# Kernel tuning notes

Hardware: AMD Instinct MI355X
Metric: run time of the kernel (lower is better)

Reference implementation:

```python
import jax, jax.numpy as jnp
import numpy as np

TAU = 1.5      # lif_tau
V_TH = 1.0     # spikingjelly default v_threshold
EPS = 1e-5     # BatchNorm eps
ALPHA = 4.0    # spikingjelly default sigmoid surrogate alpha

@jax.custom_vjp
def spike_fn(x):
    return (x >= 0.0).astype(x.dtype)

def _spike_fwd(x):
    return spike_fn(x), x

def _spike_bwd(x, g):
    s = jax.nn.sigmoid(ALPHA * x)
    return (g * ALPHA * s * (1.0 - s),)

spike_fn.defvjp(_spike_fwd, _spike_bwd)

def lif(x):
    # x: [T, B, C, N]; hard reset to 0, decay_input=True, detach_reset=True
    def step(v, xt):
        v = v + (xt - v) / TAU
        s = spike_fn(v - V_TH)
        sd = jax.lax.stop_gradient(s)
        v = (1.0 - sd) * v
        return v, s
    _, spikes = jax.lax.scan(step, jnp.zeros_like(x[0]), x)
    return spikes

def bn(x, gamma, beta, mean, var):
    # eval-mode BatchNorm1d over channel dim of [B, C, L]
    inv = gamma * jax.lax.rsqrt(var + EPS)
    return x * inv[None, :, None] + (beta - mean * inv)[None, :, None]

def setup_inputs() -> dict:
    key = jax.random.key(0)
    ks = jax.random.split(key, 13)
    B, C, T, N, H = 8, 256, 4, 4096, 1024
    return {
        "x": jax.random.normal(ks[0], (B, C, T, N), jnp.float32),
        "fc1_w": jax.random.normal(ks[1], (H, C), jnp.float32) * 0.05,
        "fc1_b": jax.random.normal(ks[2], (H,), jnp.float32) * 0.05,
        "fc2_w": jax.random.normal(ks[3], (C, H), jnp.float32) * 0.05,
        "fc2_b": jax.random.normal(ks[4], (C,), jnp.float32) * 0.05,
        "bn1_gamma": jax.random.uniform(ks[5], (H,), jnp.float32, 0.5, 1.5),
        "bn1_beta": jax.random.normal(ks[6], (H,), jnp.float32) * 0.1,
        "bn1_mean": jax.random.normal(ks[7], (H,), jnp.float32) * 0.1,
        "bn1_var": jax.random.uniform(ks[8], (H,), jnp.float32, 0.5, 1.5),
        "bn2_gamma": jax.random.uniform(ks[9], (C,), jnp.float32, 0.5, 1.5),
        "bn2_beta": jax.random.normal(ks[10], (C,), jnp.float32) * 0.1,
        "bn2_mean": jax.random.normal(ks[11], (C,), jnp.float32) * 0.1,
        "bn2_var": jax.random.uniform(ks[12], (C,), jnp.float32, 0.5, 1.5),
    }

def reference(x, fc1_w, fc1_b, fc2_w, fc2_b,
              bn1_gamma, bn1_beta, bn1_mean, bn1_var,
              bn2_gamma, bn2_beta, bn2_mean, bn2_var):
    B, C, T, N = x.shape
    H = fc1_w.shape[0]
    # fc2_bn on raw input, then LIF over T
    h = bn(x.reshape(B, C, T * N), bn2_gamma, bn2_beta, bn2_mean, bn2_var)
    h = h.reshape(B, C, T, N).transpose(2, 0, 1, 3)          # [T,B,C,N]
    h = lif(h).transpose(1, 2, 0, 3).reshape(B, C, T * N)    # [B,C,TN]
    # fc1: 1x1 conv == GEMM over channels
    h = jnp.einsum('hc,bcl->bhl', fc1_w, h) + fc1_b[None, :, None]
    h = bn(h, bn1_gamma, bn1_beta, bn1_mean, bn1_var)
    h = h.reshape(B, H, T, N).transpose(2, 0, 1, 3)          # [T,B,H,N]
    h = lif(h).transpose(1, 2, 0, 3).reshape(B, H, T * N)    # [B,H,TN]
    # fc2
    h = jnp.einsum('ch,bhl->bcl', fc2_w, h) + fc2_b[None, :, None]
    return h.reshape(B, C, T, N)
```

## Files before the change

kernel.cpp:

```cpp
#include <hip/hip_runtime.h>

#define BB 8
#define CC 256
#define TT 4
#define NNv 4096
#define HH 1024
#define LLv (TT*NNv)

typedef int int4v __attribute__((ext_vector_type(4)));

static __device__ __forceinline__ void barrier_keep_vmem() {
    asm volatile("s_waitcnt lgkmcnt(0)" ::: "memory");
    __builtin_amdgcn_s_barrier();
    __builtin_amdgcn_sched_barrier(0);
}

__global__ __launch_bounds__(256) void k_prep1(const float* __restrict__ w,
                                               unsigned char* __restrict__ wd)
{
    int i = blockIdx.x * 256 + threadIdx.x;
    int h = i >> 8, c = i & 255;
    int w24 = __float2int_rn(w[i] * 16777216.0f);
    int d2 = ((w24 + 128) & 255) - 128;  w24 = (w24 - d2) >> 8;
    int d1 = ((w24 + 128) & 255) - 128;  w24 = (w24 - d1) >> 8;
    int d0 = w24;
    size_t off = ((((size_t)(h >> 6) * 4 + (c >> 6)) * 4 + ((h >> 4) & 3)) << 10)
               + ((c >> 4) & 3) * 256 + (h & 15) * 16 + (c & 15);
    wd[off] = (unsigned char)d0;
    wd[262144 + off] = (unsigned char)d1;
    wd[2 * 262144 + off] = (unsigned char)d2;
}

__global__ __launch_bounds__(256) void k_prep2(const float* __restrict__ w,
                                               unsigned char* __restrict__ wd)
{
    int i = blockIdx.x * 256 + threadIdx.x;
    int c = i >> 10, h = i & 1023;
    int w16 = __float2int_rn(w[i] * 65536.0f);
    int d1 = ((w16 + 128) & 255) - 128;  w16 = (w16 - d1) >> 8;
    int d0 = w16;
    size_t off = ((((((size_t)(c >> 6) * 8 + (h >> 7)) * 2 + ((h >> 6) & 1)) * 4
                    + ((c >> 4) & 3)) << 10)
                 + ((h >> 4) & 3) * 256 + (c & 15) * 16 + (h & 15));
    wd[off] = (unsigned char)d0;
    wd[262144 + off] = (unsigned char)d1;
}

__global__ __launch_bounds__(256) void k_bn2_lif_t(
    const float* __restrict__ x,
    const float* __restrict__ g, const float* __restrict__ be,
    const float* __restrict__ mu, const float* __restrict__ va,
    unsigned char* __restrict__ s1T, int b0)
{
    __shared__ unsigned char ts[TT][64][80];
    int tx = threadIdx.x;
    int n0 = blockIdx.x * 64;
    int c0 = blockIdx.y * 64;
    int bl = blockIdx.z;
    int b  = b0 + bl;
    int cl = tx >> 2, np = tx & 3;
    int c = c0 + cl;
    float rsq = __fdiv_rn(1.0f, __fsqrt_rn(__fadd_rn(va[c], 1e-5f)));
    float inv = __fmul_rn(g[c], rsq);
    float add = __fsub_rn(be[c], __fmul_rn(mu[c], inv));
    size_t xb = ((size_t)(b * CC + c) * TT) * NNv + n0 + np * 16;
    float v[16];
    #pragma unroll
    for (int i = 0; i < 16; i++) v[i] = 0.0f;
    #pragma unroll
    for (int t = 0; t < TT; t++) {
        float4 p[4];
        #pragma unroll
        for (int k = 0; k < 4; k++) p[k] = *(const float4*)(x + xb + (size_t)t * NNv + 4 * k);
        const float* xp = (const float*)p;
        unsigned int ob[4] = {0, 0, 0, 0};
        #pragma unroll
        for (int i = 0; i < 16; i++) {
            float y = __fadd_rn(__fmul_rn(xp[i], inv), add);
            float vv = __fadd_rn(v[i], __fdiv_rn(__fsub_rn(y, v[i]), 1.5f));
            bool sp = vv >= 1.0f;
            v[i] = sp ? 0.0f : vv;
            if (sp) ob[i >> 2] |= 1u << (8 * (i & 3));
        }
        uint4 pk; pk.x = ob[0]; pk.y = ob[1]; pk.z = ob[2]; pk.w = ob[3];
        *(uint4*)&ts[t][cl][np * 16] = pk;
    }
    __syncthreads();
    int nl = tx >> 2, cp = tx & 3;
    #pragma unroll
    for (int t = 0; t < TT; t++) {
        unsigned int u[4];
        #pragma unroll
        for (int kk = 0; kk < 4; kk++) {
            u[kk] = (unsigned int)ts[t][cp * 16 + kk * 4 + 0][nl]
                  | ((unsigned int)ts[t][cp * 16 + kk * 4 + 1][nl] << 8)
                  | ((unsigned int)ts[t][cp * 16 + kk * 4 + 2][nl] << 16)
                  | ((unsigned int)ts[t][cp * 16 + kk * 4 + 3][nl] << 24);
        }
        uint4 pk; pk.x = u[0]; pk.y = u[1]; pk.z = u[2]; pk.w = u[3];
        *(uint4*)(s1T + ((size_t)(bl * TT + t) * NNv + n0 + nl) * CC + c0 + cp * 16) = pk;
    }
}

__global__ __launch_bounds__(256, 3) void k_gemm1_lif(
    const unsigned char* __restrict__ w1d,
    const float* __restrict__ b1,
    const float* __restrict__ g1, const float* __restrict__ be1,
    const float* __restrict__ mu1, const float* __restrict__ va1,
    const unsigned char* __restrict__ s1T, unsigned char* __restrict__ s2T)
{
    __shared__ unsigned char Lsraw[TT * 32 * 80];
    const int tx = threadIdx.x;
    const int n0 = blockIdx.x * 32;
    const int ht = blockIdx.y;
    const int bl = blockIdx.z;
    const int lane = tx & 63, w = tx >> 6;
    const int q = lane >> 4, ln = lane & 15;
    const int mh = (w & 1) * 32, wn = (w >> 1) * 16;
    const int h0 = ht * 64;

    int4v a0[TT][2], a1[TT][2], a2[TT][2];
    #pragma unroll
    for (int t = 0; t < TT; t++)
    #pragma unroll
    for (int mi = 0; mi < 2; mi++) {
        a0[t][mi] = (int4v){0, 0, 0, 0};
        a1[t][mi] = (int4v){0, 0, 0, 0};
        a2[t][mi] = (int4v){0, 0, 0, 0};
    }

    unsigned long long d[2][4];
    #pragma unroll
    for (int i = 0; i < 4; i++) {
        int task = i * 256 + tx;
        int cb = task & 7, nr = (task >> 3) & 31, t = task >> 8;
        d[0][i] = *(const unsigned long long*)(
            s1T + ((size_t)(bl * TT + t) * NNv + n0 + nr) * CC + 0 * 64 + cb * 8);
    }

    #pragma unroll
    for (int ko = 0; ko < 4; ko++) {
        const int cur = ko & 1;
        if (ko > 0) barrier_keep_vmem();
        #pragma unroll
        for (int i = 0; i < 4; i++) {
            int task = i * 256 + tx;
            int cb = task & 7, nr = (task >> 3) & 31, t = task >> 8;
            *(unsigned long long*)(Lsraw + (t * 32 + nr) * 80 + cb * 8) = d[cur][i];
        }
        if (ko < 3) {
            #pragma unroll
            for (int i = 0; i < 4; i++) {
                int task = i * 256 + tx;
                int cb = task & 7, nr = (task >> 3) & 31, t = task >> 8;
                d[cur ^ 1][i] = *(const unsigned long long*)(
                    s1T + ((size_t)(bl * TT + t) * NNv + n0 + nr) * CC + (ko + 1) * 64 + cb * 8);
            }
        }
        int4v w0[2], w1[2], w2[2];
        #pragma unroll
        for (int mi = 0; mi < 2; mi++) {
            size_t fb = ((((size_t)ht * 4 + ko) * 4 + (mh >> 4) + mi) << 10) + lane * 16;
            w0[mi] = *(const int4v*)(w1d + fb);
            w1[mi] = *(const int4v*)(w1d + 262144 + fb);
            w2[mi] = *(const int4v*)(w1d + 2 * 262144 + fb);
        }
        barrier_keep_vmem();

        int4v sf[TT];
        #pragma unroll
        for (int t = 0; t < TT; t++)
            sf[t] = *(const int4v*)(Lsraw + (t * 32 + wn + ln) * 80 + q * 16);
        #pragma unroll
        for (int t = 0; t < TT; t++)
        #pragma unroll
        for (int mi = 0; mi < 2; mi++) {
            a0[t][mi] = __builtin_amdgcn_mfma_i32_16x16x64_i8(w0[mi], sf[t], a0[t][mi], 0, 0, 0);
            a1[t][mi] = __builtin_amdgcn_mfma_i32_16x16x64_i8(w1[mi], sf[t], a1[t][mi], 0, 0, 0);
            a2[t][mi] = __builtin_amdgcn_mfma_i32_16x16x64_i8(w2[mi], sf[t], a2[t][mi], 0, 0, 0);
        }
    }

    barrier_keep_vmem();

    const int l_loc = wn + ln;
    #pragma unroll
    for (int mi = 0; mi < 2; mi++) {
        float invr[4], addr_[4], biasr[4];
        #pragma unroll
        for (int r = 0; r < 4; r++) {
            int h = h0 + mh + mi * 16 + q * 4 + r;
            float rsq = __fdiv_rn(1.0f, __fsqrt_rn(__fadd_rn(va1[h], 1e-5f)));
            invr[r] = __fmul_rn(g1[h], rsq);
            addr_[r] = __fsub_rn(be1[h], __fmul_rn(mu1[h], invr[r]));
            biasr[r] = b1[h];
        }
        float v4[4] = {0.f, 0.f, 0.f, 0.f};
        #pragma unroll
        for (int t = 0; t < TT; t++) {
            int4v ci = (((a0[t][mi] << 8) + a1[t][mi]) << 8) + a2[t][mi];
            unsigned int pk = 0;
            #pragma unroll
            for (int r = 0; r < 4; r++) {
                float h1 = __fadd_rn(__fmul_rn((float)ci[r], 5.9604644775390625e-08f),
                                     biasr[r]);
                float y  = __fadd_rn(__fmul_rn(h1, invr[r]), addr_[r]);
                float vv = __fadd_rn(v4[r], __fdiv_rn(__fsub_rn(y, v4[r]), 1.5f));
                bool sp = vv >= 1.0f;
                v4[r] = sp ? 0.0f : vv;
                if (sp) pk |= (1u << (8 * r));
            }
            *(unsigned int*)(Lsraw + (t * 32 + l_loc) * 80
                             + ((mh >> 2) + mi * 4 + q) * 4) = pk;
        }
    }
    __syncthreads();

    #pragma unroll
    for (int p = 0; p < 2; p++) {
        int task = p * 256 + tx;
        int t = task >> 7, l = (task >> 2) & 31, ch = task & 3;
        uint4 vv = *(const uint4*)(Lsraw + (t * 32 + l) * 80 + ch * 16);
        *(uint4*)(s2T + ((size_t)bl * LLv + t * NNv + n0 + l) * HH + h0 + ch * 16) = vv;
    }
}

__global__ __launch_bounds__(256, 3) void k_gemm2(
    const unsigned char* __restrict__ w2d,
    const float* __restrict__ b2c,
    const unsigned char* __restrict__ s2T, float* __restrict__ outp, int b0)
{
    __shared__ unsigned char Ls[64][144];
    const int tx = threadIdx.x;
    const int l0 = blockIdx.x * 64;
    const int ct = blockIdx.y;
    const int bl = blockIdx.z;
    const int b  = b0 + bl;
    const int lane = tx & 63, w = tx >> 6;
    const int q = lane >> 4, ln = lane & 15;
    const int mc = w * 32;

    int4v a0[2][4], a1[2][4];
    #pragma unroll
    for (int mi = 0; mi < 2; mi++)
    #pragma unroll
    for (int ni = 0; ni < 4; ni++) {
        a0[mi][ni] = (int4v){0, 0, 0, 0};
        a1[mi][ni] = (int4v){0, 0, 0, 0};
    }

    unsigned long long d[2][4];
    #pragma unroll
    for (int i = 0; i < 4; i++) {
        int task = i * 256 + tx;
        int hb = task & 15, lr = task >> 4;
        d[0][i] = *(const unsigned long long*)(
            s2T + ((size_t)bl * LLv + l0 + lr) * HH + 0 * 128 + hb * 8);
    }

    #pragma unroll
    for (int ko = 0; ko < 8; ko++) {
        const int cur = ko & 1;
        if (ko > 0) barrier_keep_vmem();
        #pragma unroll
        for (int i = 0; i < 4; i++) {
            int task = i * 256 + tx;
            int hb = task & 15, lr = task >> 4;
            *(unsigned long long*)&Ls[lr][hb * 8] = d[cur][i];
        }
        if (ko < 7) {
            #pragma unroll
            for (int i = 0; i < 4; i++) {
                int task = i * 256 + tx;
                int hb = task & 15, lr = task >> 4;
                d[cur ^ 1][i] = *(const unsigned long long*)(
                    s2T + ((size_t)bl * LLv + l0 + lr) * HH + (ko + 1) * 128 + hb * 8);
            }
        }
        int4v w0[2][2], w1[2][2];
        #pragma unroll
        for (int kb = 0; kb < 2; kb++)
        #pragma unroll
        for (int mi = 0; mi < 2; mi++) {
            size_t fb = (((((size_t)(ct * 2 + (w >> 1)) * 8 + ko) * 2 + kb) * 4
                          + (w & 1) * 2 + mi) << 10) + lane * 16;
            w0[kb][mi] = *(const int4v*)(w2d + fb);
            w1[kb][mi] = *(const int4v*)(w2d + 262144 + fb);
        }
        barrier_keep_vmem();

        #pragma unroll
        for (int kb = 0; kb < 2; kb++) {
            int4v sf[4];
            #pragma unroll
            for (int ni = 0; ni < 4; ni++)
                sf[ni] = *(const int4v*)&Ls[ni * 16 + ln][kb * 64 + q * 16];
            #pragma unroll
            for (int mi = 0; mi < 2; mi++)
            #pragma unroll
            for (int ni = 0; ni < 4; ni++) {
                a0[mi][ni] = __builtin_amdgcn_mfma_i32_16x16x64_i8(w0[kb][mi], sf[ni], a0[mi][ni], 0, 0, 0);
                a1[mi][ni] = __builtin_amdgcn_mfma_i32_16x16x64_i8(w1[kb][mi], sf[ni], a1[mi][ni], 0, 0, 0);
            }
        }
    }
    #pragma unroll
    for (int mi = 0; mi < 2; mi++)
    #pragma unroll
    for (int ni = 0; ni < 4; ni++) {
        int4v tv = (a0[mi][ni] << 8) + a1[mi][ni];
        #pragma unroll
        for (int r = 0; r < 4; r++) {
            int c = ct * 128 + mc + mi * 16 + q * 4 + r;
            int l = l0 + ni * 16 + ln;
            outp[((size_t)b * CC + c) * LLv + l] =
                __fadd_rn(__fmul_rn((float)tv[r], 1.52587890625e-05f), b2c[c]);
        }
    }
}

extern "C" void kernel_launch(void* const* d_in, const int* in_sizes, int n_in,
                              void* d_out, int out_size, void* d_ws, size_t ws_size,
                              hipStream_t stream) {
    const float* x    = (const float*)d_in[0];
    const float* fc1w = (const float*)d_in[1];
    const float* fc1b = (const float*)d_in[2];
    const float* fc2w = (const float*)d_in[3];
    const float* fc2b = (const float*)d_in[4];
    const float* g1   = (const float*)d_in[5];
    const float* be1  = (const float*)d_in[6];
    const float* mu1  = (const float*)d_in[7];
    const float* va1  = (const float*)d_in[8];
    const float* g2   = (const float*)d_in[9];
    const float* be2  = (const float*)d_in[10];
    const float* mu2  = (const float*)d_in[11];
    const float* va2  = (const float*)d_in[12];

    const size_t WB  = (size_t)3 * 262144 + (size_t)2 * 262144;
    const size_t S1B = (size_t)TT * NNv * CC;
    const size_t S2B = (size_t)LLv * HH;

    int nbc;
    bool full_s1;
    if      (ws_size >= WB + 8 * S1B + 8 * S2B) { nbc = 8; full_s1 = true;  }
    else if (ws_size >= WB + 8 * S1B + 4 * S2B) { nbc = 4; full_s1 = true;  }
    else if (ws_size >= WB + 8 * S1B + 2 * S2B) { nbc = 2; full_s1 = true;  }
    else if (ws_size >= WB + 8 * S1B + 1 * S2B) { nbc = 1; full_s1 = true;  }
    else                                        { nbc = 1; full_s1 = false; }

    unsigned char* w1d = (unsigned char*)d_ws;
    unsigned char* w2d = w1d + (size_t)3 * 262144;
    unsigned char* s1T = w2d + (size_t)2 * 262144;
    unsigned char* s2T = s1T + (full_s1 ? (size_t)8 * S1B : S1B);
    float* outp = (float*)d_out;

    hipLaunchKernelGGL(k_prep1, dim3(1024), dim3(256), 0, stream, fc1w, w1d);
    hipLaunchKernelGGL(k_prep2, dim3(1024), dim3(256), 0, stream, fc2w, w2d);

    if (full_s1) {
        hipLaunchKernelGGL(k_bn2_lif_t, dim3(NNv / 64, CC / 64, BB), dim3(256), 0, stream,
                           x, g2, be2, mu2, va2, s1T, 0);
        for (int b0 = 0; b0 < BB; b0 += nbc) {
            hipLaunchKernelGGL(k_gemm1_lif, dim3(NNv / 32, HH / 64, nbc), dim3(256), 0, stream,
                               w1d, fc1b, g1, be1, mu1, va1, s1T + (size_t)b0 * S1B, s2T);
            hipLaunchKernelGGL(k_gemm2, dim3(LLv / 64, CC / 128, nbc), dim3(256), 0, stream,
                               w2d, fc2b, s2T, outp, b0);
        }
    } else {
        for (int b0 = 0; b0 < BB; ++b0) {
            hipLaunchKernelGGL(k_bn2_lif_t, dim3(NNv / 64, CC / 64, 1), dim3(256), 0, stream,
                               x, g2, be2, mu2, va2, s1T, b0);
            hipLaunchKernelGGL(k_gemm1_lif, dim3(NNv / 32, HH / 64, 1), dim3(256), 0, stream,
                               w1d, fc1b, g1, be1, mu1, va1, s1T, s2T);
            hipLaunchKernelGGL(k_gemm2, dim3(LLv / 64, CC / 128, 1), dim3(256), 0, stream,
                               w2d, fc2b, s2T, outp, b0);
        }
    }
}
```

Baseline: 542.9 us.

## Stage full-K activation tiles in LDS and loop over output tiles inside each block

gemm1 now loads the whole 256-channel spike tile for 32 positions into LDS once and loops over all 16 hidden tiles in-block, with BN constants precomputed into shared memory. Its output s2T moves to an h-tile-major layout ([b][ht][L][64]) that it writes directly from registers. gemm2 now loads the full 1024-deep spike tile into LDS once and loops over both channel tiles, and the per-K-step double-buffered barriers are dropped. The aim is to avoid re-reading activations once per output tile, at the cost of larger LDS, fewer blocks, and weight loads that are no longer software-pipelined.

```diff
diff --git a/kernel.cpp b/kernel.cpp
--- a/kernel.cpp
+++ b/kernel.cpp
@@ -8,12 +8,6 @@
 #define LLv (TT*NNv)
 
 typedef int int4v __attribute__((ext_vector_type(4)));
-
-static __device__ __forceinline__ void barrier_keep_vmem() {
-    asm volatile("s_waitcnt lgkmcnt(0)" ::: "memory");
-    __builtin_amdgcn_s_barrier();
-    __builtin_amdgcn_sched_barrier(0);
-}
 
 __global__ __launch_bounds__(256) void k_prep1(const float* __restrict__ w,
                                                unsigned char* __restrict__ wd)
@@ -102,103 +96,87 @@
     }
 }
 
-__global__ __launch_bounds__(256, 3) void k_gemm1_lif(
+
+__global__ __launch_bounds__(512, 4) void k_gemm1_lif(
     const unsigned char* __restrict__ w1d,
     const float* __restrict__ b1,
     const float* __restrict__ g1, const float* __restrict__ be1,
     const float* __restrict__ mu1, const float* __restrict__ va1,
     const unsigned char* __restrict__ s1T, unsigned char* __restrict__ s2T)
 {
-    __shared__ unsigned char Lsraw[TT * 32 * 80];
+    __shared__ unsigned char Ls[128][272];
+    __shared__ float Linv[HH], Ladd[HH], Lbias[HH];
     const int tx = threadIdx.x;
     const int n0 = blockIdx.x * 32;
-    const int ht = blockIdx.y;
     const int bl = blockIdx.z;
     const int lane = tx & 63, w = tx >> 6;
     const int q = lane >> 4, ln = lane & 15;
-    const int mh = (w & 1) * 32, wn = (w >> 1) * 16;
-    const int h0 = ht * 64;
-
-    int4v a0[TT][2], a1[TT][2], a2[TT][2];
-    #pragma unroll
-    for (int t = 0; t < TT; t++)
-    #pragma unroll
-    for (int mi = 0; mi < 2; mi++) {
-        a0[t][mi] = (int4v){0, 0, 0, 0};
-        a1[t][mi] = (int4v){0, 0, 0, 0};
-        a2[t][mi] = (int4v){0, 0, 0, 0};
-    }
-
-    unsigned long long d[2][4];
-    #pragma unroll
-    for (int i = 0; i < 4; i++) {
-        int task = i * 256 + tx;
-        int cb = task & 7, nr = (task >> 3) & 31, t = task >> 8;
-        d[0][i] = *(const unsigned long long*)(
-            s1T + ((size_t)(bl * TT + t) * NNv + n0 + nr) * CC + 0 * 64 + cb * 8);
-    }
-
-    #pragma unroll
-    for (int ko = 0; ko < 4; ko++) {
-        const int cur = ko & 1;
-        if (ko > 0) barrier_keep_vmem();
+    const int mh = (w & 3) * 16;
+    const int wn = (w >> 2) * 16;
+
+    #pragma unroll
+    for (int rep = 0; rep < 2; rep++) {
+        int hh = rep * 512 + tx;
+        float rsq = __fdiv_rn(1.0f, __fsqrt_rn(__fadd_rn(va1[hh], 1e-5f)));
+        float inv = __fmul_rn(g1[hh], rsq);
+        Linv[hh] = inv;
+        Ladd[hh] = __fsub_rn(be1[hh], __fmul_rn(mu1[hh], inv));
+        Lbias[hh] = b1[hh];
+    }
+    {
+        uint4 st[4];
         #pragma unroll
         for (int i = 0; i < 4; i++) {
-            int task = i * 256 + tx;
-            int cb = task & 7, nr = (task >> 3) & 31, t = task >> 8;
-            *(unsigned long long*)(Lsraw + (t * 32 + nr) * 80 + cb * 8) = d[cur][i];
-        }
-        if (ko < 3) {
-            #pragma unroll
-            for (int i = 0; i < 4; i++) {
-                int task = i * 256 + tx;
-                int cb = task & 7, nr = (task >> 3) & 31, t = task >> 8;
-                d[cur ^ 1][i] = *(const unsigned long long*)(
-                    s1T + ((size_t)(bl * TT + t) * NNv + n0 + nr) * CC + (ko + 1) * 64 + cb * 8);
-            }
-        }
-        int4v w0[2], w1[2], w2[2];
-        #pragma unroll
-        for (int mi = 0; mi < 2; mi++) {
-            size_t fb = ((((size_t)ht * 4 + ko) * 4 + (mh >> 4) + mi) << 10) + lane * 16;
-            w0[mi] = *(const int4v*)(w1d + fb);
-            w1[mi] = *(const int4v*)(w1d + 262144 + fb);
-            w2[mi] = *(const int4v*)(w1d + 2 * 262144 + fb);
-        }
-        barrier_keep_vmem();
-
-        int4v sf[TT];
-        #pragma unroll
-        for (int t = 0; t < TT; t++)
-            sf[t] = *(const int4v*)(Lsraw + (t * 32 + wn + ln) * 80 + q * 16);
-        #pragma unroll
-        for (int t = 0; t < TT; t++)
-        #pragma unroll
-        for (int mi = 0; mi < 2; mi++) {
-            a0[t][mi] = __builtin_amdgcn_mfma_i32_16x16x64_i8(w0[mi], sf[t], a0[t][mi], 0, 0, 0);
-            a1[t][mi] = __builtin_amdgcn_mfma_i32_16x16x64_i8(w1[mi], sf[t], a1[t][mi], 0, 0, 0);
-            a2[t][mi] = __builtin_amdgcn_mfma_i32_16x16x64_i8(w2[mi], sf[t], a2[t][mi], 0, 0, 0);
-        }
-    }
-
-    barrier_keep_vmem();
-
-    const int l_loc = wn + ln;
-    #pragma unroll
-    for (int mi = 0; mi < 2; mi++) {
+            int task = i * 512 + tx;
+            int ch = task & 15, row = task >> 4;
+            st[i] = *(const uint4*)(s1T + ((size_t)(bl * TT + (row >> 5)) * NNv
+                                           + n0 + (row & 31)) * CC + ch * 16);
+        }
+        #pragma unroll
+        for (int i = 0; i < 4; i++) {
+            int task = i * 512 + tx;
+            int ch = task & 15, row = task >> 4;
+            *(uint4*)&Ls[row][ch * 16] = st[i];
+        }
+    }
+    __syncthreads();
+
+    for (int ht = 0; ht < 16; ht++) {
+        int4v a0[TT], a1[TT], a2[TT];
+        #pragma unroll
+        for (int t = 0; t < TT; t++) {
+            a0[t] = (int4v){0, 0, 0, 0};
+            a1[t] = (int4v){0, 0, 0, 0};
+            a2[t] = (int4v){0, 0, 0, 0};
+        }
+        #pragma unroll
+        for (int ko = 0; ko < 4; ko++) {
+            size_t fb = ((((size_t)ht * 4 + ko) * 4 + (w & 3)) << 10) + lane * 16;
+            int4v w0 = *(const int4v*)(w1d + fb);
+            int4v w1 = *(const int4v*)(w1d + 262144 + fb);
+            int4v w2 = *(const int4v*)(w1d + 2 * 262144 + fb);
+            int4v sf[TT];
+            #pragma unroll
+            for (int t = 0; t < TT; t++)
+                sf[t] = *(const int4v*)&Ls[t * 32 + wn + ln][ko * 64 + q * 16];
+            #pragma unroll
+            for (int t = 0; t < TT; t++) {
+                a0[t] = __builtin_amdgcn_mfma_i32_16x16x64_i8(w0, sf[t], a0[t], 0, 0, 0);
+                a1[t] = __builtin_amdgcn_mfma_i32_16x16x64_i8(w1, sf[t], a1[t], 0, 0, 0);
+                a2[t] = __builtin_amdgcn_mfma_i32_16x16x64_i8(w2, sf[t], a2[t], 0, 0, 0);
+            }
+        }
         float invr[4], addr_[4], biasr[4];
         #pragma unroll
         for (int r = 0; r < 4; r++) {
-            int h = h0 + mh + mi * 16 + q * 4 + r;
-            float rsq = __fdiv_rn(1.0f, __fsqrt_rn(__fadd_rn(va1[h], 1e-5f)));
-            invr[r] = __fmul_rn(g1[h], rsq);
-            addr_[r] = __fsub_rn(be1[h], __fmul_rn(mu1[h], invr[r]));
-            biasr[r] = b1[h];
+            int h = ht * 64 + mh + q * 4 + r;
+            invr[r] = Linv[h]; addr_[r] = Ladd[h]; biasr[r] = Lbias[h];
         }
         float v4[4] = {0.f, 0.f, 0.f, 0.f};
+        const int nloc = n0 + wn + ln;
         #pragma unroll
         for (int t = 0; t < TT; t++) {
-            int4v ci = (((a0[t][mi] << 8) + a1[t][mi]) << 8) + a2[t][mi];
+            int4v ci = (((a0[t] << 8) + a1[t]) << 8) + a2[t];
             unsigned int pk = 0;
             #pragma unroll
             for (int r = 0; r < 4; r++) {
@@ -210,111 +188,90 @@
                 v4[r] = sp ? 0.0f : vv;
                 if (sp) pk |= (1u << (8 * r));
             }
-            *(unsigned int*)(Lsraw + (t * 32 + l_loc) * 80
-                             + ((mh >> 2) + mi * 4 + q) * 4) = pk;
-        }
-    }
-    __syncthreads();
-
-    #pragma unroll
-    for (int p = 0; p < 2; p++) {
-        int task = p * 256 + tx;
-        int t = task >> 7, l = (task >> 2) & 31, ch = task & 3;
-        uint4 vv = *(const uint4*)(Lsraw + (t * 32 + l) * 80 + ch * 16);
-        *(uint4*)(s2T + ((size_t)bl * LLv + t * NNv + n0 + l) * HH + h0 + ch * 16) = vv;
-    }
-}
-
-__global__ __launch_bounds__(256, 3) void k_gemm2(
+            *(unsigned int*)(s2T + ((((size_t)(bl * 16 + ht) * LLv + t * NNv + nloc)) << 6)
+                             + mh + q * 4) = pk;
+        }
+    }
+}
+
+__global__ __launch_bounds__(256, 2) void k_gemm2(
     const unsigned char* __restrict__ w2d,
     const float* __restrict__ b2c,
     const unsigned char* __restrict__ s2T, float* __restrict__ outp, int b0)
 {
-    __shared__ unsigned char Ls[64][144];
+    __shared__ unsigned char Ls[64][1040];
     const int tx = threadIdx.x;
     const int l0 = blockIdx.x * 64;
-    const int ct = blockIdx.y;
     const int bl = blockIdx.z;
     const int b  = b0 + bl;
     const int lane = tx & 63, w = tx >> 6;
     const int q = lane >> 4, ln = lane & 15;
     const int mc = w * 32;
 
-    int4v a0[2][4], a1[2][4];
-    #pragma unroll
-    for (int mi = 0; mi < 2; mi++)
-    #pragma unroll
-    for (int ni = 0; ni < 4; ni++) {
-        a0[mi][ni] = (int4v){0, 0, 0, 0};
-        a1[mi][ni] = (int4v){0, 0, 0, 0};
-    }
-
-    unsigned long long d[2][4];
-    #pragma unroll
-    for (int i = 0; i < 4; i++) {
-        int task = i * 256 + tx;
-        int hb = task & 15, lr = task >> 4;
-        d[0][i] = *(const unsigned long long*)(
-            s2T + ((size_t)bl * LLv + l0 + lr) * HH + 0 * 128 + hb * 8);
-    }
-
-    #pragma unroll
-    for (int ko = 0; ko < 8; ko++) {
-        const int cur = ko & 1;
-        if (ko > 0) barrier_keep_vmem();
-        #pragma unroll
-        for (int i = 0; i < 4; i++) {
-            int task = i * 256 + tx;
-            int hb = task & 15, lr = task >> 4;
-            *(unsigned long long*)&Ls[lr][hb * 8] = d[cur][i];
-        }
-        if (ko < 7) {
-            #pragma unroll
-            for (int i = 0; i < 4; i++) {
-                int task = i * 256 + tx;
-                int hb = task & 15, lr = task >> 4;
-                d[cur ^ 1][i] = *(const unsigned long long*)(
-                    s2T + ((size_t)bl * LLv + l0 + lr) * HH + (ko + 1) * 128 + hb * 8);
-            }
-        }
-        int4v w0[2][2], w1[2][2];
-        #pragma unroll
-        for (int kb = 0; kb < 2; kb++)
-        #pragma unroll
-        for (int mi = 0; mi < 2; mi++) {
-            size_t fb = (((((size_t)(ct * 2 + (w >> 1)) * 8 + ko) * 2 + kb) * 4
-                          + (w & 1) * 2 + mi) << 10) + lane * 16;
-            w0[kb][mi] = *(const int4v*)(w2d + fb);
-            w1[kb][mi] = *(const int4v*)(w2d + 262144 + fb);
-        }
-        barrier_keep_vmem();
-
+    #pragma unroll
+    for (int half = 0; half < 2; half++) {
+        uint4 st[8];
+        #pragma unroll
+        for (int i = 0; i < 8; i++) {
+            int task = half * 2048 + i * 256 + tx;
+            int lr = task >> 6, ch = task & 63;
+            st[i] = *(const uint4*)(s2T + ((size_t)(bl * 16 + (ch >> 2)) * LLv
+                                           + l0 + lr) * 64 + (ch & 3) * 16);
+        }
+        #pragma unroll
+        for (int i = 0; i < 8; i++) {
+            int task = half * 2048 + i * 256 + tx;
+            int lr = task >> 6, ch = task & 63;
+            *(uint4*)&Ls[lr][ch * 16] = st[i];
+        }
+    }
+    __syncthreads();
+
+    for (int ct = 0; ct < 2; ct++) {
+        int4v a0[2][4], a1[2][4];
+        #pragma unroll
+        for (int mi = 0; mi < 2; mi++)
+        #pragma unroll
+        for (int ni = 0; ni < 4; ni++) {
+            a0[mi][ni] = (int4v){0, 0, 0, 0};
+            a1[mi][ni] = (int4v){0, 0, 0, 0};
+        }
+        #pragma unroll
+        for (int ko = 0; ko < 8; ko++)
         #pragma unroll
         for (int kb = 0; kb < 2; kb++) {
+            int4v w0[2], w1[2];
+            #pragma unroll
+            for (int mi = 0; mi < 2; mi++) {
+                size_t fb = (((((size_t)(ct * 2 + (w >> 1)) * 8 + ko) * 2 + kb) * 4
+                              + (w & 1) * 2 + mi) << 10) + lane * 16;
+                w0[mi] = *(const int4v*)(w2d + fb);
+                w1[mi] = *(const int4v*)(w2d + 262144 + fb);
+            }
             int4v sf[4];
             #pragma unroll
             for (int ni = 0; ni < 4; ni++)
-                sf[ni] = *(const int4v*)&Ls[ni * 16 + ln][kb * 64 + q * 16];
+                sf[ni] = *(const int4v*)&Ls[ni * 16 + ln][ko * 128 + kb * 64 + q * 16];
             #pragma unroll
             for (int mi = 0; mi < 2; mi++)
             #pragma unroll
             for (int ni = 0; ni < 4; ni++) {
-                a0[mi][ni] = __builtin_amdgcn_mfma_i32_16x16x64_i8(w0[kb][mi], sf[ni], a0[mi][ni], 0, 0, 0);
-                a1[mi][ni] = __builtin_amdgcn_mfma_i32_16x16x64_i8(w1[kb][mi], sf[ni], a1[mi][ni], 0, 0, 0);
-            }
-        }
-    }
-    #pragma unroll
-    for (int mi = 0; mi < 2; mi++)
-    #pragma unroll
-    for (int ni = 0; ni < 4; ni++) {
-        int4v tv = (a0[mi][ni] << 8) + a1[mi][ni];
-        #pragma unroll
-        for (int r = 0; r < 4; r++) {
-            int c = ct * 128 + mc + mi * 16 + q * 4 + r;
-            int l = l0 + ni * 16 + ln;
-            outp[((size_t)b * CC + c) * LLv + l] =
-                __fadd_rn(__fmul_rn((float)tv[r], 1.52587890625e-05f), b2c[c]);
+                a0[mi][ni] = __builtin_amdgcn_mfma_i32_16x16x64_i8(w0[mi], sf[ni], a0[mi][ni], 0, 0, 0);
+                a1[mi][ni] = __builtin_amdgcn_mfma_i32_16x16x64_i8(w1[mi], sf[ni], a1[mi][ni], 0, 0, 0);
+            }
+        }
+        #pragma unroll
+        for (int mi = 0; mi < 2; mi++)
+        #pragma unroll
+        for (int ni = 0; ni < 4; ni++) {
+            int4v tv = (a0[mi][ni] << 8) + a1[mi][ni];
+            #pragma unroll
+            for (int r = 0; r < 4; r++) {
+                int c = ct * 128 + mc + mi * 16 + q * 4 + r;
+                int l = l0 + ni * 16 + ln;
+                outp[((size_t)b * CC + c) * LLv + l] =
+                    __fadd_rn(__fmul_rn((float)tv[r], 1.52587890625e-05f), b2c[c]);
+            }
         }
     }
 }
@@ -361,18 +318,18 @@
         hipLaunchKernelGGL(k_bn2_lif_t, dim3(NNv / 64, CC / 64, BB), dim3(256), 0, stream,
                            x, g2, be2, mu2, va2, s1T, 0);
         for (int b0 = 0; b0 < BB; b0 += nbc) {
-            hipLaunchKernelGGL(k_gemm1_lif, dim3(NNv / 32, HH / 64, nbc), dim3(256), 0, stream,
+            hipLaunchKernelGGL(k_gemm1_lif, dim3(NNv / 32, 1, nbc), dim3(512), 0, stream,
                                w1d, fc1b, g1, be1, mu1, va1, s1T + (size_t)b0 * S1B, s2T);
-            hipLaunchKernelGGL(k_gemm2, dim3(LLv / 64, CC / 128, nbc), dim3(256), 0, stream,
+            hipLaunchKernelGGL(k_gemm2, dim3(LLv / 64, 1, nbc), dim3(256), 0, stream,
                                w2d, fc2b, s2T, outp, b0);
         }
     } else {
         for (int b0 = 0; b0 < BB; ++b0) {
             hipLaunchKernelGGL(k_bn2_lif_t, dim3(NNv / 64, CC / 64, 1), dim3(256), 0, stream,
                                x, g2, be2, mu2, va2, s1T, b0);
-            hipLaunchKernelGGL(k_gemm1_lif, dim3(NNv / 32, HH / 64, 1), dim3(256), 0, stream,
+            hipLaunchKernelGGL(k_gemm1_lif, dim3(NNv / 32, 1, 1), dim3(512), 0, stream,
                                w1d, fc1b, g1, be1, mu1, va1, s1T, s2T);
-            hipLaunchKernelGGL(k_gemm2, dim3(LLv / 64, CC / 128, 1), dim3(256), 0, stream,
+            hipLaunchKernelGGL(k_gemm2, dim3(LLv / 64, 1, 1), dim3(256), 0, stream,
                                w2d, fc2b, s2T, outp, b0);
         }
     }
```

After: 718.5 us. +32.3%, slower.
